# Optimization experiments

Hardware: AMD Instinct MI355X
Metric: run time of the kernel (lower is better)

## Reference

```python
import jax, jax.numpy as jnp
import numpy as np

PAD = 0
EPS = 1e-5


def setup_inputs() -> dict:
    key = jax.random.key(0)
    k1, k2, k3, k4, k5 = jax.random.split(key, 5)
    B, S, D, H = 16, 1024, 512, 4
    output = jax.random.normal(k1, (B, S, D), dtype=jnp.float32)
    local_cor = jax.random.normal(k2, (1,), dtype=jnp.float32)
    event_type = jax.random.randint(k3, (B, S), 0, 1000, dtype=jnp.int64)
    # xavier-ish scale for the per-layer Linear weights
    W = jax.random.normal(k4, (H, D, D), dtype=jnp.float32) * (1.0 / np.sqrt(D))
    b = jax.random.normal(k5, (H, D), dtype=jnp.float32) * 0.01
    return {"output": output, "local_cor": local_cor, "event_type": event_type, "W": W, "b": b}


def _build_mask(event_type, S, dtype):
    # subsequent mask: 1 for strictly-future positions (triu, diag=1)
    subseq = jnp.triu(jnp.ones((S, S), dtype=dtype), k=1)  # [S,S]
    # key-pad mask: 1 where key token is PAD, broadcast over query dim
    keypad = (event_type == PAD).astype(dtype)[:, None, :]  # [B,1,S]
    return ((keypad + subseq[None]) > 0).astype(dtype)  # [B,S,S]


def reference(output, local_cor, event_type, W, b):
    B, S, D = output.shape
    H = W.shape[0]
    temperature = jnp.asarray(D, output.dtype) ** 0.5
    mask = _build_mask(event_type, S, output.dtype)  # [B,S,S]

    x = output
    total = None
    for h in range(H):  # heads are applied SEQUENTIALLY in the original
        # masked QK^T scores
        attn = jnp.einsum('bqd,bkd->bqk', x / temperature, x) * mask  # [B,S,S]
        # L2 normalize along keys (F.normalize p=2, eps=1e-5)
        norm = jnp.sqrt(jnp.sum(attn * attn, axis=-1, keepdims=True))
        attn = attn / jnp.maximum(norm, EPS)
        # value path: ELU(Linear(x))
        v = jax.nn.elu(jnp.einsum('bsd,ed->bse', x, W[h]) + b[h])  # [B,S,D]
        x = jnp.einsum('bqk,bkd->bqd', attn, v)
        total = x if total is None else total + x
    return total
```

## Files before the change

kernel.cpp:

```cpp
#include <hip/hip_runtime.h>
#include <math.h>

#define B_ 16
#define S_ 1024
#define D_ 512
#define H_ 4
#define INV_TEMP 0.044194173824159216f
#define C_SCALE 0.00390625f
#define OUT_SCALE 256.0f

typedef _Float16 f16;
typedef _Float16 f16x8 __attribute__((ext_vector_type(8)));
typedef _Float16 f16x4 __attribute__((ext_vector_type(4)));
typedef float f32x4 __attribute__((ext_vector_type(4)));

#define AS1(p) ((const __attribute__((address_space(1))) void*)(p))
#define AS3(p) ((__attribute__((address_space(3))) void*)(p))
#define MFMA __builtin_amdgcn_mfma_f32_16x16x32_f16

__global__ __launch_bounds__(256)
void k_pre(const float* __restrict__ x0, f16* __restrict__ xh,
           const float* __restrict__ W, f16* __restrict__ Wh,
           const int* __restrict__ etype, int* __restrict__ flag,
           float* __restrict__ ssb)
{
    const int t = threadIdx.x;
    const int bi = blockIdx.x;
    if (bi < 8192) {
        const int i = bi * 256 + t;
        const float4 v = ((const float4*)x0)[i];
        f16x4 h; h[0] = (f16)v.x; h[1] = (f16)v.y; h[2] = (f16)v.z; h[3] = (f16)v.w;
        ((f16x4*)xh)[i] = h;
    } else if (bi < 9216) {
        const int i = (bi - 8192) * 256 + t;
        const float4 v = ((const float4*)W)[i];
        f16x4 h; h[0] = (f16)v.x; h[1] = (f16)v.y; h[2] = (f16)v.z; h[3] = (f16)v.w;
        ((f16x4*)Wh)[i] = h;
    } else if (bi == 9216) {
        if (t < 128) {
            const int b = t >> 3, kt = t & 7;
            const int* p = etype + b * S_ + kt * 128;
            int any0 = 0;
#pragma unroll
            for (int i = 0; i < 128; i += 4) {
                const int4 v = *(const int4*)(p + i);
                any0 |= (v.x == 0) | (v.y == 0) | (v.z == 0) | (v.w == 0);
            }
            flag[t] = any0;
        }
    } else {
        const int i = (bi - 9217) * 256 + t;
        ((float4*)ssb)[i] = make_float4(0.f, 0.f, 0.f, 0.f);
    }
}

__device__ __forceinline__ void stage128x64(const f16* __restrict__ src, int ld,
                                            char* lds0, int t)
{
    const int r = t >> 3;
    const int c = ((t & 7) ^ (r & 7)) << 3;
    const f16* g = src + (size_t)r * ld + c;
#pragma unroll
    for (int j = 0; j < 4; ++j)
        __builtin_amdgcn_global_load_lds(AS1(g + (size_t)(32 * j) * ld),
                                         AS3(lds0 + j * 4096 + t * 16), 16, 0, 0);
}

__device__ __forceinline__ void mma64(const char* ldsA, const char* ldsB,
                                      int wm, int wn, int lr, int quad,
                                      f32x4 (*acc)[4])
{
#pragma unroll
    for (int kk = 0; kk < 2; ++kk) {
        f16x8 af[4], bf[4];
#pragma unroll
        for (int i = 0; i < 4; ++i) {
            const int row = wm * 64 + i * 16 + lr;
            af[i] = *(const f16x8*)(ldsA + (row << 7) +
                                    ((((kk << 2) + quad) ^ (row & 7)) << 4));
        }
#pragma unroll
        for (int j = 0; j < 4; ++j) {
            const int row = wn * 64 + j * 16 + lr;
            bf[j] = *(const f16x8*)(ldsB + (row << 7) +
                                    ((((kk << 2) + quad) ^ (row & 7)) << 4));
        }
#pragma unroll
        for (int i = 0; i < 4; ++i)
#pragma unroll
            for (int j = 0; j < 4; ++j)
                acc[i][j] = MFMA(af[i], bf[j], acc[i][j], 0, 0, 0);
    }
}

__device__ __forceinline__ void gemm_core64(const f16* A, int ldA,
                                            const f16* Bm, int ldB,
                                            int K, char* lds, int t,
                                            int wm, int wn, int lr, int quad,
                                            f32x4 (*acc)[4], bool diag)
{
    char* lb = diag ? lds : lds + 16384;
    for (int k0 = 0; k0 < K; k0 += 64) {
        stage128x64(A + k0, ldA, lds, t);
        if (!diag) stage128x64(Bm + k0, ldB, lb, t);
        __syncthreads();
        mma64(lds, lb, wm, wn, lr, quad, acc);
        __syncthreads();
    }
}

__global__ __launch_bounds__(256)
void k_vs(const f16* __restrict__ xh, const f16* __restrict__ Wh,
          const float* __restrict__ bias, f16* __restrict__ vT,
          const int* __restrict__ etype, const int* __restrict__ flag,
          f16* __restrict__ sh, float* __restrict__ ss)
{
    __shared__ __align__(16) char lds[32768];
    const int t = threadIdx.x;
    const int w = t >> 6, lane = t & 63, lr = lane & 15, quad = lane >> 4;
    const int wm = w & 1, wn = w >> 1;

    if (blockIdx.x < 1024) {
        const int i0 = blockIdx.x;
        const int xcd = i0 & 7, j0 = i0 >> 3;
        const int b = 2 * xcd + (j0 & 1);
        const int tile = j0 >> 1;
        const int bk = (tile & 7) * 128;
        const int bq = (tile >> 3) * 128;
        if (bk < bq && !flag[b * 8 + (bk >> 7)]) return;

        const f16* xb = xh + (size_t)b * S_ * D_;
        f32x4 acc[4][4] = {};
        gemm_core64(xb + (size_t)bk * D_, D_, xb + (size_t)bq * D_, D_, D_,
                    lds, t, wm, wn, lr, quad, acc, bk == bq);
        const float sc = INV_TEMP * C_SCALE;
        float ssq[4] = {0.0f, 0.0f, 0.0f, 0.0f};
#pragma unroll
        for (int i = 0; i < 4; ++i) {
            const int k4 = bk + wm * 64 + i * 16 + quad * 4;
            const int4 et = *(const int4*)(etype + b * S_ + k4);
            const int ev[4] = {et.x, et.y, et.z, et.w};
#pragma unroll
            for (int j = 0; j < 4; ++j) {
                const int q = bq + wn * 64 + j * 16 + lr;
                f16x4 hv;
#pragma unroll
                for (int r = 0; r < 4; ++r) {
                    const bool keep = ((k4 + r) > q) || (ev[r] == 0);
                    hv[r] = (f16)(keep ? acc[i][j][r] * sc : 0.0f);
                    const float fv = (float)hv[r];
                    ssq[j] += fv * fv;
                }
                *(f16x4*)(sh + ((size_t)b * S_ + q) * S_ + k4) = hv;
            }
        }
#pragma unroll
        for (int j = 0; j < 4; ++j) {
            float v = ssq[j];
            v += __shfl_xor(v, 16, 64);
            v += __shfl_xor(v, 32, 64);
            if (quad == 0) {
                const int q = bq + wn * 64 + j * 16 + lr;
                atomicAdd(ss + b * S_ + q, v);
            }
        }
    } else {
        const int idx = blockIdx.x - 1024;
        const int bm = (idx & 127) * 128;
        const int bn = (idx >> 7) * 128;
        f32x4 acc[4][4] = {};
        gemm_core64(xh + (size_t)bm * D_, D_, Wh + (size_t)bn * D_, D_, D_,
                    lds, t, wm, wn, lr, quad, acc, false);
#pragma unroll
        for (int j = 0; j < 4; ++j) {
            const int e = bn + wn * 64 + j * 16 + lr;
            const float be = bias[e];
#pragma unroll
            for (int i = 0; i < 4; ++i) {
                const int m = bm + wm * 64 + i * 16 + quad * 4;
                const int batch = m >> 10, s = m & 1023;
                f16x4 hv;
#pragma unroll
                for (int r = 0; r < 4; ++r) {
                    float z = acc[i][j][r] + be;
                    z = (z > 0.0f) ? z : (expf(z) - 1.0f);
                    hv[r] = (f16)z;
                }
                *(f16x4*)(vT + ((size_t)batch * D_ + e) * S_ + s) = hv;
            }
        }
    }
}

__global__ __launch_bounds__(512)
void k_out(const f16* __restrict__ vT, const f16* __restrict__ sh,
           const float* __restrict__ ss, const int* __restrict__ flag,
           f16* __restrict__ xh_w,
           const f16* __restrict__ xs0, const f16* __restrict__ xs1,
           const f16* __restrict__ xs2,
           float* __restrict__ out, const int accum, const int wout)
{
    __shared__ __align__(16) char lds[65536];
    __shared__ int klist[32];
    __shared__ int kcnt;
    const int t = threadIdx.x;
    const int g = t >> 8;
    const int tl = t & 255;
    const int w = tl >> 6, lane = tl & 63, lr = lane & 15, quad = lane >> 4;
    const int wm = w & 1, wn = w >> 1;
    const int i0 = blockIdx.x;
    const int xcd = i0 & 7, j0 = i0 >> 3;
    const int b = 2 * xcd + (j0 & 1);
    const int tile = j0 >> 1;
    const int be = (tile & 3) * 128;
    const int bq = (tile >> 2) * 128;
    const int qt = bq >> 7;

    if (t == 0) {
        int n = 0;
        for (int kc = 0; kc < 8; ++kc)
            if (kc >= qt || flag[b * 8 + kc]) {
                const int kb = kc * 128;
                klist[n] = kb; klist[n + 1] = kb + 32;
                klist[n + 2] = kb + 64; klist[n + 3] = kb + 96;
                n += 4;
            }
        kcnt = n;
    }
    __syncthreads();
    const int half = kcnt >> 1;
    const int s0 = g ? half : 0;

    const f16* Abase = vT + ((size_t)b * D_ + be) * S_;
    const f16* Bbase = sh + ((size_t)b * S_ + bq) * S_;
    char* myl = lds + (g << 15);
    f32x4 acc[4][4] = {};
#pragma unroll 1
    for (int i = 0; i < half; i += 2) {
        const int k0 = klist[s0 + i];
        stage128x64(Abase + k0, S_, myl, tl);
        stage128x64(Bbase + k0, S_, myl + 16384, tl);
        __syncthreads();
        mma64(myl, myl + 16384, wm, wn, lr, quad, acc);
        __syncthreads();
    }

    if (g == 1) {
#pragma unroll
        for (int j = 0; j < 4; ++j)
#pragma unroll
            for (int i = 0; i < 4; ++i)
                *(f32x4*)(lds + (((w * 16 + j * 4 + i) * 64 + lane) << 4)) = acc[i][j];
    }
    __syncthreads();
    if (g == 0) {
#pragma unroll
        for (int j = 0; j < 4; ++j) {
            const int q = bq + wn * 64 + j * 16 + lr;
            const float ssv = ss[b * S_ + q];
            const float scl = 1.0f / (C_SCALE * fmaxf(sqrtf(ssv) * OUT_SCALE, 1e-5f));
#pragma unroll
            for (int i = 0; i < 4; ++i) {
                const f32x4 other =
                    *(const f32x4*)(lds + (((w * 16 + j * 4 + i) * 64 + lane) << 4));
                const f32x4 sum = acc[i][j] + other;
                const int e4 = be + wm * 64 + i * 16 + quad * 4;
                const size_t o = ((size_t)b * S_ + q) * D_ + e4;
                f32x4 val;
                f16x4 hx;
#pragma unroll
                for (int r = 0; r < 4; ++r) {
                    val[r] = sum[r] * scl;
                    hx[r] = (f16)val[r];
                }
                if (xh_w) *(f16x4*)(xh_w + o) = hx;
                if (xs0) {
                    const f16x4 a0 = *(const f16x4*)(xs0 + o);
                    const f16x4 a1 = *(const f16x4*)(xs1 + o);
                    const f16x4 a2 = *(const f16x4*)(xs2 + o);
#pragma unroll
                    for (int r = 0; r < 4; ++r)
                        val[r] += (float)a0[r] + (float)a1[r] + (float)a2[r];
                }
                if (wout) {
                    f32x4 v2 = val;
                    if (accum) { const f32x4 old = *(const f32x4*)(out + o); v2 = v2 + old; }
                    *(f32x4*)(out + o) = v2;
                }
            }
        }
    }
}

extern "C" void kernel_launch(void* const* d_in, const int* in_sizes, int n_in,
                              void* d_out, int out_size, void* d_ws, size_t ws_size,
                              hipStream_t stream) {
    const float* x0    = (const float*)d_in[0];
    const int*   etype = (const int*)d_in[2];
    const float* W     = (const float*)d_in[3];
    const float* bias  = (const float*)d_in[4];
    float* out = (float*)d_out;

    char* ws = (char*)d_ws;
    f16*   xA    = (f16*)(ws);
    f16*   vT    = (f16*)(ws + (16u << 20));
    f16*   sh    = (f16*)(ws + (32u << 20));
    f16*   Wh    = (f16*)(ws + (64u << 20));
    float* ssb   = (float*)(ws + (66u << 20));
    int*   flags = (int*)(ws + (66u << 20) + 262144);

    const bool big = ws_size >= ((size_t)101 << 20);
    f16* xB = big ? (f16*)(ws + (68u << 20)) : xA;
    f16* xC = big ? (f16*)(ws + (84u << 20)) : xA;

    k_pre<<<9281, 256, 0, stream>>>(x0, xA, W, Wh, etype, flags, ssb);

    f16* xin[H_]  = {xA, xA, xB, xC};
    f16* xdst[H_] = {xA, xB, xC, nullptr};

    for (int h = 0; h < H_; ++h) {
        float* ss = ssb + (size_t)h * B_ * S_;
        k_vs <<<1536, 256, 0, stream>>>(xin[h], Wh + (size_t)h * D_ * D_,
                                        bias + (size_t)h * D_, vT,
                                        etype, flags, sh, ss);
        if (big) {
            const bool last = (h == H_ - 1);
            k_out<<<512, 512, 0, stream>>>(vT, sh, ss, flags, xdst[h],
                                           last ? xA : nullptr,
                                           last ? xB : nullptr,
                                           last ? xC : nullptr,
                                           out, 0, last ? 1 : 0);
        } else {
            k_out<<<512, 512, 0, stream>>>(vT, sh, ss, flags,
                                           (h < H_ - 1) ? xA : nullptr,
                                           nullptr, nullptr, nullptr,
                                           out, h > 0, 1);
        }
    }
}
```

Measured before the change: 339.1 us.

## Enlarge k_vs GEMM tiles to 128x256 with 512-thread blocks

Both GEMM paths in k_vs (masked scores and the V projection) now use 128x256 output tiles computed by 8 waves in 512-thread blocks, with dedicated staging helpers. This halves the block count and raises operand reuse per LDS load. The diagonal-tile special case is dropped, so diagonal score tiles now stage both operands, and LDS per block grows to 48KB, which may lower occupancy. Tiles are skipped only when they lie entirely below the causal boundary and the flag is clear.

```diff
diff --git a/kernel.cpp b/kernel.cpp
--- a/kernel.cpp
+++ b/kernel.cpp
@@ -66,6 +66,29 @@
                                          AS3(lds0 + j * 4096 + t * 16), 16, 0, 0);
 }
 
+__device__ __forceinline__ void stageA128_512(const f16* __restrict__ src, int ld,
+                                              char* lds0, int t)
+{
+    const int r = t >> 3;
+    const int c = ((t & 7) ^ (r & 7)) << 3;
+    const f16* g = src + (size_t)r * ld + c;
+    __builtin_amdgcn_global_load_lds(AS1(g), AS3(lds0 + t * 16), 16, 0, 0);
+    __builtin_amdgcn_global_load_lds(AS1(g + (size_t)64 * ld),
+                                     AS3(lds0 + 8192 + t * 16), 16, 0, 0);
+}
+
+__device__ __forceinline__ void stageB256_512(const f16* __restrict__ src, int ld,
+                                              char* lds0, int t)
+{
+    const int r = t >> 3;
+    const int c = ((t & 7) ^ (r & 7)) << 3;
+    const f16* g = src + (size_t)r * ld + c;
+#pragma unroll
+    for (int j = 0; j < 4; ++j)
+        __builtin_amdgcn_global_load_lds(AS1(g + (size_t)(64 * j) * ld),
+                                         AS3(lds0 + j * 8192 + t * 16), 16, 0, 0);
+}
+
 __device__ __forceinline__ void mma64(const char* ldsA, const char* ldsB,
                                       int wm, int wn, int lr, int quad,
                                       f32x4 (*acc)[4])
@@ -93,46 +116,37 @@
     }
 }
 
-__device__ __forceinline__ void gemm_core64(const f16* A, int ldA,
-                                            const f16* Bm, int ldB,
-                                            int K, char* lds, int t,
-                                            int wm, int wn, int lr, int quad,
-                                            f32x4 (*acc)[4], bool diag)
-{
-    char* lb = diag ? lds : lds + 16384;
-    for (int k0 = 0; k0 < K; k0 += 64) {
-        stage128x64(A + k0, ldA, lds, t);
-        if (!diag) stage128x64(Bm + k0, ldB, lb, t);
-        __syncthreads();
-        mma64(lds, lb, wm, wn, lr, quad, acc);
-        __syncthreads();
-    }
-}
-
-__global__ __launch_bounds__(256)
+__global__ __launch_bounds__(512)
 void k_vs(const f16* __restrict__ xh, const f16* __restrict__ Wh,
           const float* __restrict__ bias, f16* __restrict__ vT,
           const int* __restrict__ etype, const int* __restrict__ flag,
           f16* __restrict__ sh, float* __restrict__ ss)
 {
-    __shared__ __align__(16) char lds[32768];
+    __shared__ __align__(16) char lds[49152];
     const int t = threadIdx.x;
-    const int w = t >> 6, lane = t & 63, lr = lane & 15, quad = lane >> 4;
-    const int wm = w & 1, wn = w >> 1;
-
-    if (blockIdx.x < 1024) {
+    const int lane = t & 63, lr = lane & 15, quad = lane >> 4;
+    const int w = t >> 6, wm = w >> 2, wn = w & 3;
+
+    if (blockIdx.x < 512) {
         const int i0 = blockIdx.x;
         const int xcd = i0 & 7, j0 = i0 >> 3;
         const int b = 2 * xcd + (j0 & 1);
         const int tile = j0 >> 1;
-        const int bk = (tile & 7) * 128;
-        const int bq = (tile >> 3) * 128;
-        if (bk < bq && !flag[b * 8 + (bk >> 7)]) return;
+        const int kt = tile & 7, qt2 = tile >> 3;
+        if (kt < 2 * qt2 && !flag[b * 8 + kt]) return;
+        const int bk = kt * 128, bq = qt2 * 256;
 
         const f16* xb = xh + (size_t)b * S_ * D_;
+        const f16* A  = xb + (size_t)bk * D_;
+        const f16* Bm = xb + (size_t)bq * D_;
         f32x4 acc[4][4] = {};
-        gemm_core64(xb + (size_t)bk * D_, D_, xb + (size_t)bq * D_, D_, D_,
-                    lds, t, wm, wn, lr, quad, acc, bk == bq);
+        for (int k0 = 0; k0 < D_; k0 += 64) {
+            stageA128_512(A + k0, D_, lds, t);
+            stageB256_512(Bm + k0, D_, lds + 16384, t);
+            __syncthreads();
+            mma64(lds, lds + 16384, wm, wn, lr, quad, acc);
+            __syncthreads();
+        }
         const float sc = INV_TEMP * C_SCALE;
         float ssq[4] = {0.0f, 0.0f, 0.0f, 0.0f};
 #pragma unroll
@@ -165,20 +179,25 @@
             }
         }
     } else {
-        const int idx = blockIdx.x - 1024;
+        const int idx = blockIdx.x - 512;
         const int bm = (idx & 127) * 128;
-        const int bn = (idx >> 7) * 128;
+        const int bn = (idx >> 7) * 256;
+        const int b = bm >> 10;
         f32x4 acc[4][4] = {};
-        gemm_core64(xh + (size_t)bm * D_, D_, Wh + (size_t)bn * D_, D_, D_,
-                    lds, t, wm, wn, lr, quad, acc, false);
+        for (int k0 = 0; k0 < D_; k0 += 64) {
+            stageA128_512(xh + (size_t)bm * D_ + k0, D_, lds, t);
+            stageB256_512(Wh + (size_t)bn * D_ + k0, D_, lds + 16384, t);
+            __syncthreads();
+            mma64(lds, lds + 16384, wm, wn, lr, quad, acc);
+            __syncthreads();
+        }
 #pragma unroll
         for (int j = 0; j < 4; ++j) {
             const int e = bn + wn * 64 + j * 16 + lr;
             const float be = bias[e];
 #pragma unroll
             for (int i = 0; i < 4; ++i) {
-                const int m = bm + wm * 64 + i * 16 + quad * 4;
-                const int batch = m >> 10, s = m & 1023;
+                const int s = (bm & 1023) + wm * 64 + i * 16 + quad * 4;
                 f16x4 hv;
 #pragma unroll
                 for (int r = 0; r < 4; ++r) {
@@ -186,7 +205,7 @@
                     z = (z > 0.0f) ? z : (expf(z) - 1.0f);
                     hv[r] = (f16)z;
                 }
-                *(f16x4*)(vT + ((size_t)batch * D_ + e) * S_ + s) = hv;
+                *(f16x4*)(vT + ((size_t)b * D_ + e) * S_ + s) = hv;
             }
         }
     }
@@ -320,9 +339,9 @@
 
     for (int h = 0; h < H_; ++h) {
         float* ss = ssb + (size_t)h * B_ * S_;
-        k_vs <<<1536, 256, 0, stream>>>(xin[h], Wh + (size_t)h * D_ * D_,
-                                        bias + (size_t)h * D_, vT,
-                                        etype, flags, sh, ss);
+        k_vs <<<768, 512, 0, stream>>>(xin[h], Wh + (size_t)h * D_ * D_,
+                                       bias + (size_t)h * D_, vT,
+                                       etype, flags, sh, ss);
         if (big) {
             const bool last = (h == H_ - 1);
             k_out<<<512, 512, 0, stream>>>(vT, sh, ss, flags, xdst[h],
```

Measured after the change: 336.9 us. No clear change (-0.6%).

## Double-buffer k_vs GEMM staging with explicit waitcnt and XCD-aware block mapping

Applied to the files above, without the earlier changes.

Replaces the single-buffered GEMM loop in k_vs with a double-buffered pipeline that prefetches the next K-slice into a second LDS buffer while MFMAs run on the current one. It uses explicit vmcnt/lgkmcnt waits, sched barriers and inline ds_read_b128 with precomputed swizzled offsets. The block-to-batch mapping in k_pre and the value GEMM is remapped so each XCD works on the same batches, improving L2 locality. The diagonal score tile no longer shares A and B staging, LDS per block doubles to 64KB (lower occupancy), and the hand-written waitcnt counts must match the number of outstanding loads exactly.

```diff
diff --git a/kernel.cpp b/kernel.cpp
--- a/kernel.cpp
+++ b/kernel.cpp
@@ -18,6 +18,26 @@
 #define AS3(p) ((__attribute__((address_space(3))) void*)(p))
 #define MFMA __builtin_amdgcn_mfma_f32_16x16x32_f16
 
+#define SBAR()                                                                 \
+    do {                                                                       \
+        __builtin_amdgcn_sched_barrier(0);                                     \
+        __builtin_amdgcn_s_barrier();                                          \
+        __builtin_amdgcn_sched_barrier(0);                                     \
+    } while (0)
+#define VMF(N)                                                                 \
+    do {                                                                       \
+        __builtin_amdgcn_sched_barrier(0);                                     \
+        asm volatile("s_waitcnt vmcnt(" #N ")" ::: "memory");                  \
+        __builtin_amdgcn_sched_barrier(0);                                     \
+    } while (0)
+
+__device__ __forceinline__ f16x8 ds_rd16(unsigned addr)
+{
+    f16x8 r;
+    asm volatile("ds_read_b128 %0, %1" : "=v"(r) : "v"(addr));
+    return r;
+}
+
 __global__ __launch_bounds__(256)
 void k_pre(const float* __restrict__ x0, f16* __restrict__ xh,
            const float* __restrict__ W, f16* __restrict__ Wh,
@@ -27,7 +47,10 @@
     const int t = threadIdx.x;
     const int bi = blockIdx.x;
     if (bi < 8192) {
-        const int i = bi * 256 + t;
+        const int xcd = bi & 7, j = bi >> 3;
+        const int b = 2 * xcd + (j & 1);
+        const int off = j >> 1;
+        const int i = (b * 512 + off) * 256 + t;
         const float4 v = ((const float4*)x0)[i];
         f16x4 h; h[0] = (f16)v.x; h[1] = (f16)v.y; h[2] = (f16)v.z; h[3] = (f16)v.w;
         ((f16x4*)xh)[i] = h;
@@ -66,47 +89,61 @@
                                          AS3(lds0 + j * 4096 + t * 16), 16, 0, 0);
 }
 
-__device__ __forceinline__ void mma64(const char* ldsA, const char* ldsB,
-                                      int wm, int wn, int lr, int quad,
-                                      f32x4 (*acc)[4])
-{
+__device__ __forceinline__ void mma_asm(unsigned aB, unsigned bB,
+                                        const unsigned (*offA)[2],
+                                        const unsigned (*offB)[2],
+                                        f32x4 (*acc)[4])
+{
+    f16x8 af[4][2], bf[4][2];
 #pragma unroll
     for (int kk = 0; kk < 2; ++kk) {
-        f16x8 af[4], bf[4];
-#pragma unroll
-        for (int i = 0; i < 4; ++i) {
-            const int row = wm * 64 + i * 16 + lr;
-            af[i] = *(const f16x8*)(ldsA + (row << 7) +
-                                    ((((kk << 2) + quad) ^ (row & 7)) << 4));
-        }
-#pragma unroll
-        for (int j = 0; j < 4; ++j) {
-            const int row = wn * 64 + j * 16 + lr;
-            bf[j] = *(const f16x8*)(ldsB + (row << 7) +
-                                    ((((kk << 2) + quad) ^ (row & 7)) << 4));
-        }
+#pragma unroll
+        for (int i = 0; i < 4; ++i) af[i][kk] = ds_rd16(aB + offA[i][kk]);
+#pragma unroll
+        for (int j = 0; j < 4; ++j) bf[j][kk] = ds_rd16(bB + offB[j][kk]);
+    }
+    asm volatile("s_waitcnt lgkmcnt(0)" ::: "memory");
+    __builtin_amdgcn_sched_barrier(0);
+#pragma unroll
+    for (int kk = 0; kk < 2; ++kk)
 #pragma unroll
         for (int i = 0; i < 4; ++i)
 #pragma unroll
             for (int j = 0; j < 4; ++j)
-                acc[i][j] = MFMA(af[i], bf[j], acc[i][j], 0, 0, 0);
-    }
-}
-
-__device__ __forceinline__ void gemm_core64(const f16* A, int ldA,
-                                            const f16* Bm, int ldB,
-                                            int K, char* lds, int t,
-                                            int wm, int wn, int lr, int quad,
-                                            f32x4 (*acc)[4], bool diag)
-{
-    char* lb = diag ? lds : lds + 16384;
-    for (int k0 = 0; k0 < K; k0 += 64) {
-        stage128x64(A + k0, ldA, lds, t);
-        if (!diag) stage128x64(Bm + k0, ldB, lb, t);
-        __syncthreads();
-        mma64(lds, lb, wm, wn, lr, quad, acc);
-        __syncthreads();
-    }
+                acc[i][j] = MFMA(af[i][kk], bf[j][kk], acc[i][j], 0, 0, 0);
+}
+
+__device__ __forceinline__ void gemm_cnt(const f16* __restrict__ A, int ldA,
+                                         const f16* __restrict__ Bm, int ldB,
+                                         char* lds, int t,
+                                         const unsigned (*offA)[2],
+                                         const unsigned (*offB)[2],
+                                         f32x4 (*acc)[4])
+{
+    const unsigned base = (unsigned)(unsigned long long)AS3(lds);
+    stage128x64(A, ldA, lds, t);
+    stage128x64(Bm, ldB, lds + 16384, t);
+#pragma unroll 1
+    for (int i = 0; i < 3; ++i) {
+        const int k1 = i * 128 + 64, k2 = i * 128 + 128;
+        stage128x64(A + k1, ldA, lds + 32768, t);
+        stage128x64(Bm + k1, ldB, lds + 49152, t);
+        VMF(8); SBAR();
+        mma_asm(base, base + 16384, offA, offB, acc);
+        SBAR();
+        stage128x64(A + k2, ldA, lds, t);
+        stage128x64(Bm + k2, ldB, lds + 16384, t);
+        VMF(8); SBAR();
+        mma_asm(base + 32768, base + 49152, offA, offB, acc);
+        SBAR();
+    }
+    stage128x64(A + 448, ldA, lds + 32768, t);
+    stage128x64(Bm + 448, ldB, lds + 49152, t);
+    VMF(8); SBAR();
+    mma_asm(base, base + 16384, offA, offB, acc);
+    SBAR();
+    VMF(0); SBAR();
+    mma_asm(base + 32768, base + 49152, offA, offB, acc);
 }
 
 __global__ __launch_bounds__(256)
@@ -115,10 +152,22 @@
           const int* __restrict__ etype, const int* __restrict__ flag,
           f16* __restrict__ sh, float* __restrict__ ss)
 {
-    __shared__ __align__(16) char lds[32768];
+    __shared__ __align__(16) char lds[65536];
     const int t = threadIdx.x;
     const int w = t >> 6, lane = t & 63, lr = lane & 15, quad = lane >> 4;
     const int wm = w & 1, wn = w >> 1;
+
+    unsigned offA[4][2], offB[4][2];
+#pragma unroll
+    for (int i = 0; i < 4; ++i) {
+        const int ra = wm * 64 + i * 16 + lr;
+        const int rb = wn * 64 + i * 16 + lr;
+#pragma unroll
+        for (int kk = 0; kk < 2; ++kk) {
+            offA[i][kk] = (unsigned)((ra << 7) + ((((kk << 2) + quad) ^ (ra & 7)) << 4));
+            offB[i][kk] = (unsigned)((rb << 7) + ((((kk << 2) + quad) ^ (rb & 7)) << 4));
+        }
+    }
 
     if (blockIdx.x < 1024) {
         const int i0 = blockIdx.x;
@@ -131,8 +180,8 @@
 
         const f16* xb = xh + (size_t)b * S_ * D_;
         f32x4 acc[4][4] = {};
-        gemm_core64(xb + (size_t)bk * D_, D_, xb + (size_t)bq * D_, D_, D_,
-                    lds, t, wm, wn, lr, quad, acc, bk == bq);
+        gemm_cnt(xb + (size_t)bk * D_, D_, xb + (size_t)bq * D_, D_,
+                 lds, t, offA, offB, acc);
         const float sc = INV_TEMP * C_SCALE;
         float ssq[4] = {0.0f, 0.0f, 0.0f, 0.0f};
 #pragma unroll
@@ -166,19 +215,22 @@
         }
     } else {
         const int idx = blockIdx.x - 1024;
-        const int bm = (idx & 127) * 128;
-        const int bn = (idx >> 7) * 128;
+        const int xcd = idx & 7;
+        const int b = 2 * xcd + ((idx >> 3) & 1);
+        const int rest = idx >> 4;
+        const int sq = rest & 7;
+        const int bn = (rest >> 3) * 128;
+        const int bm = b * 1024 + sq * 128;
         f32x4 acc[4][4] = {};
-        gemm_core64(xh + (size_t)bm * D_, D_, Wh + (size_t)bn * D_, D_, D_,
-                    lds, t, wm, wn, lr, quad, acc, false);
+        gemm_cnt(xh + (size_t)bm * D_, D_, Wh + (size_t)bn * D_, D_,
+                 lds, t, offA, offB, acc);
 #pragma unroll
         for (int j = 0; j < 4; ++j) {
             const int e = bn + wn * 64 + j * 16 + lr;
             const float be = bias[e];
 #pragma unroll
             for (int i = 0; i < 4; ++i) {
-                const int m = bm + wm * 64 + i * 16 + quad * 4;
-                const int batch = m >> 10, s = m & 1023;
+                const int s = sq * 128 + wm * 64 + i * 16 + quad * 4;
                 f16x4 hv;
 #pragma unroll
                 for (int r = 0; r < 4; ++r) {
@@ -186,9 +238,36 @@
                     z = (z > 0.0f) ? z : (expf(z) - 1.0f);
                     hv[r] = (f16)z;
                 }
-                *(f16x4*)(vT + ((size_t)batch * D_ + e) * S_ + s) = hv;
-            }
-        }
+                *(f16x4*)(vT + ((size_t)b * D_ + e) * S_ + s) = hv;
+            }
+        }
+    }
+}
+
+__device__ __forceinline__ void mma64(const char* ldsA, const char* ldsB,
+                                      int wm, int wn, int lr, int quad,
+                                      f32x4 (*acc)[4])
+{
+#pragma unroll
+    for (int kk = 0; kk < 2; ++kk) {
+        f16x8 af[4], bf[4];
+#pragma unroll
+        for (int i = 0; i < 4; ++i) {
+            const int row = wm * 64 + i * 16 + lr;
+            af[i] = *(const f16x8*)(ldsA + (row << 7) +
+                                    ((((kk << 2) + quad) ^ (row & 7)) << 4));
+        }
+#pragma unroll
+        for (int j = 0; j < 4; ++j) {
+            const int row = wn * 64 + j * 16 + lr;
+            bf[j] = *(const f16x8*)(ldsB + (row << 7) +
+                                    ((((kk << 2) + quad) ^ (row & 7)) << 4));
+        }
+#pragma unroll
+        for (int i = 0; i < 4; ++i)
+#pragma unroll
+            for (int j = 0; j < 4; ++j)
+                acc[i][j] = MFMA(af[i], bf[j], acc[i][j], 0, 0, 0);
     }
 }
 
```

New measurement: 323.4 us. 4.6% less time.
